# Kernel tuning notes

Measured on AMD Instinct MI355X. Metric: run time of the kernel, lower is better.

The kernel has to match this reference:

```python
import jax, jax.numpy as jnp
import numpy as np
import math

HIDDEN = 1024
HEADS = 16
HEAD_DIM = HIDDEN // HEADS
RANK = 16
LORA_SCALING = 1.0 / RANK  # loralib default lora_alpha=1 -> scaling = alpha/r


def setup_inputs() -> dict:
    key = jax.random.key(0)
    ks = jax.random.split(key, 16)
    bs, seq = 4, 2048
    inp = {
        "hidden_states": jax.random.normal(ks[0], (bs, seq, HIDDEN), dtype=jnp.float32),
        "attention_mask": jnp.zeros((bs, 1, 1, seq), dtype=jnp.float32),
    }
    s = 0.02
    for i, nm in enumerate(["q", "k", "v"]):
        inp[f"W{nm}"] = jax.random.normal(ks[1 + 4 * i], (HIDDEN, HIDDEN), dtype=jnp.float32) * s
        inp[f"b{nm}"] = jnp.zeros((HIDDEN,), dtype=jnp.float32)
        inp[f"A{nm}"] = jax.random.normal(ks[2 + 4 * i], (RANK, HIDDEN), dtype=jnp.float32) * s
        inp[f"B{nm}"] = jnp.zeros((HIDDEN, RANK), dtype=jnp.float32)  # loralib inits B to zero
    return inp


def _lora_linear(x, W, b, A, B):
    # y = x W^T + b + scaling * (x A^T) B^T
    return x @ W.T + b + LORA_SCALING * ((x @ A.T) @ B.T)


def _transform(x, W, b, A, B, bs, seq):
    proj = _lora_linear(x, W, b, A, B)  # [bs, seq, hidden]
    return proj.reshape(bs, seq, HEADS, HEAD_DIM).transpose(0, 2, 1, 3)  # [bs, h, seq, d]


def reference(hidden_states, attention_mask, Wq, bq, Aq, Bq, Wk, bk, Ak, Bk, Wv, bv, Av, Bv):
    bs, seq, _ = hidden_states.shape
    q = _transform(hidden_states, Wq, bq, Aq, Bq, bs, seq)
    k = _transform(hidden_states, Wk, bk, Ak, Bk, bs, seq)
    v = _transform(hidden_states, Wv, bv, Av, Bv, bs, seq)
    scores = jnp.einsum("bhqd,bhkd->bhqk", q, k) / math.sqrt(HEAD_DIM) + attention_mask
    probs = jax.nn.softmax(scores, axis=-1)  # [bs, h, seq, seq]
    out = jnp.einsum("bhqk,bhkd->bhqd", probs, v)  # [bs, h, seq, d]
    return out.transpose(0, 2, 1, 3).reshape(bs, seq, HIDDEN)
```

## Files before the change

### kernel.cpp

```cpp
#include <hip/hip_runtime.h>
#include <stdint.h>

typedef __bf16 bf16x8 __attribute__((ext_vector_type(8)));
typedef float f32x4 __attribute__((ext_vector_type(4)));
typedef float f32x16 __attribute__((ext_vector_type(16)));

static __device__ __forceinline__ unsigned int pk_bf16(float a, float b) {
  unsigned int d;
  asm("v_cvt_pk_bf16_f32 %0, %1, %2" : "=v"(d) : "v"(a), "v"(b));
  return d;
}
static __device__ __forceinline__ float exp2_hw(float x) {
  float r;
  asm("v_exp_f32 %0, %1" : "=v"(r) : "v"(x));
  return r;
}
static __device__ __forceinline__ float rcp_hw(float x) {
  float r;
  asm("v_rcp_f32 %0, %1" : "=v"(r) : "v"(x));
  return r;
}
static __device__ __forceinline__ void gll16(const void* g, void* l) {
  __builtin_amdgcn_global_load_lds((const __attribute__((address_space(1))) unsigned int*)g,
                                   (__attribute__((address_space(3))) unsigned int*)l,
                                   16, 0, 0);
}

__global__ __launch_bounds__(256) void prep_kernel(
    const float* __restrict__ X, unsigned short* __restrict__ Xbf,
    const float* __restrict__ Wq, const float* __restrict__ Aq, const float* __restrict__ Bq,
    const float* __restrict__ Wk, const float* __restrict__ Ak, const float* __restrict__ Bk,
    const float* __restrict__ Wv, const float* __restrict__ Av, const float* __restrict__ Bv,
    unsigned short* __restrict__ Weff) {
  int bid = blockIdx.x;
  if (bid < 8192) {
    int i = (bid * 256 + threadIdx.x) * 4;
    float4 v = *(const float4*)(X + i);
    uint2 o;
    o.x = pk_bf16(v.x, v.y);
    o.y = pk_bf16(v.z, v.w);
    *(uint2*)(Xbf + i) = o;
  } else {
    int idx = ((bid - 8192) * 256 + threadIdx.x) * 4;
    int p = idx >> 20;
    int o = (idx >> 10) & 1023;
    int i = idx & 1023;
    const float* W = (p == 0) ? Wq : (p == 1) ? Wk : Wv;
    const float* A = (p == 0) ? Aq : (p == 1) ? Ak : Av;
    const float* B = (p == 0) ? Bq : (p == 1) ? Bk : Bv;
    float4 acc = {0.f, 0.f, 0.f, 0.f};
#pragma unroll
    for (int r = 0; r < 16; ++r) {
      float bb = B[o * 16 + r];
      float4 av = *(const float4*)&A[r * 1024 + i];
      acc.x += bb * av.x; acc.y += bb * av.y;
      acc.z += bb * av.z; acc.w += bb * av.w;
    }
    float4 wv = *(const float4*)&W[o * 1024 + i];
    uint2 ov;
    ov.x = pk_bf16(wv.x + acc.x * 0.0625f, wv.y + acc.y * 0.0625f);
    ov.y = pk_bf16(wv.z + acc.z * 0.0625f, wv.w + acc.w * 0.0625f);
    *(uint2*)&Weff[idx] = ov;
  }
}

__global__ __launch_bounds__(256) void gemm_qkv(
    const unsigned short* __restrict__ X, const unsigned short* __restrict__ Weff,
    const float* __restrict__ bq, const float* __restrict__ bk, const float* __restrict__ bv,
    unsigned short* __restrict__ qbuf, unsigned short* __restrict__ kbuf,
    unsigned short* __restrict__ vtbuf) {
  __shared__ __align__(16) unsigned short As[2][128][32];
  __shared__ __align__(16) unsigned short Bs[2][128][32];
  const int K = 1024;
  int tid = threadIdx.x;
  int lane = tid & 63;
  int w = tid >> 6;
  int wm = (w >> 1) * 64;
  int wn = (w & 1) * 64;
  int c = lane & 15;
  int quad = lane >> 4;

  int bid0 = blockIdx.x;
  int bid = (bid0 & 7) * 192 + (bid0 >> 3);
  int grp = bid / 192;
  int rem = bid % 192;
  int m0 = (grp * 8 + (rem & 7)) * 128;
  int n0 = (rem >> 3) * 128;
  int p = n0 >> 10;

  int ldr = lane >> 2;
  int ldc = (lane & 3) * 8;
  const unsigned short* gA = X + (m0 + w * 32 + ldr) * K + ldc;
  const unsigned short* gB = Weff + (n0 + w * 32 + ldr) * K + ldc;

  f32x4 acc[4][4] = {};

  if (p == 2) {
    for (int k0 = 0; k0 < K; k0 += 64) {
      __syncthreads();
#pragma unroll
      for (int hh = 0; hh < 2; hh++) {
        gll16(gA + k0 + hh * 32, &As[hh][w * 32][0]);
        gll16(gA + k0 + hh * 32 + 16 * K, &As[hh][w * 32 + 16][0]);
        gll16(gB + k0 + hh * 32, &Bs[hh][w * 32][0]);
        gll16(gB + k0 + hh * 32 + 16 * K, &Bs[hh][w * 32 + 16][0]);
      }
      __syncthreads();
#pragma unroll
      for (int hh = 0; hh < 2; hh++) {
        bf16x8 af[4], bfr[4];
#pragma unroll
        for (int mi = 0; mi < 4; mi++)
          af[mi] = *(const bf16x8*)&As[hh][wm + mi * 16 + c][quad * 8];
#pragma unroll
        for (int ni = 0; ni < 4; ni++)
          bfr[ni] = *(const bf16x8*)&Bs[hh][wn + ni * 16 + c][quad * 8];
#pragma unroll
        for (int mi = 0; mi < 4; mi++)
#pragma unroll
          for (int ni = 0; ni < 4; ni++)
            acc[mi][ni] = __builtin_amdgcn_mfma_f32_16x16x32_bf16(af[mi], bfr[ni], acc[mi][ni], 0, 0, 0);
      }
    }
    const float* bias = bv;
#pragma unroll
    for (int ni = 0; ni < 4; ni++) {
      int o = (n0 + wn + ni * 16 + c) & 1023;
      int h = o >> 6;
      int d = o & 63;
      float bval = bias[o];
#pragma unroll
      for (int mi = 0; mi < 4; mi++) {
        int mbase = m0 + wm + mi * 16 + quad * 4;
        int bb = mbase >> 11;
        int s = mbase & 2047;
        uint2 o4;
        o4.x = pk_bf16(acc[mi][ni][0] + bval, acc[mi][ni][1] + bval);
        o4.y = pk_bf16(acc[mi][ni][2] + bval, acc[mi][ni][3] + bval);
        *(uint2*)&vtbuf[((bb * 16 + h) * 64 + d) * 2048 + s] = o4;
      }
    }
  } else {
    for (int k0 = 0; k0 < K; k0 += 64) {
      __syncthreads();
#pragma unroll
      for (int hh = 0; hh < 2; hh++) {
        gll16(gA + k0 + hh * 32, &As[hh][w * 32][0]);
        gll16(gA + k0 + hh * 32 + 16 * K, &As[hh][w * 32 + 16][0]);
        gll16(gB + k0 + hh * 32, &Bs[hh][w * 32][0]);
        gll16(gB + k0 + hh * 32 + 16 * K, &Bs[hh][w * 32 + 16][0]);
      }
      __syncthreads();
#pragma unroll
      for (int hh = 0; hh < 2; hh++) {
        bf16x8 af[4], bfr[4];
#pragma unroll
        for (int mi = 0; mi < 4; mi++)
          af[mi] = *(const bf16x8*)&As[hh][wm + mi * 16 + c][quad * 8];
#pragma unroll
        for (int ni = 0; ni < 4; ni++)
          bfr[ni] = *(const bf16x8*)&Bs[hh][wn + ni * 16 + c][quad * 8];
#pragma unroll
        for (int mi = 0; mi < 4; mi++)
#pragma unroll
          for (int ni = 0; ni < 4; ni++)
            acc[mi][ni] = __builtin_amdgcn_mfma_f32_16x16x32_bf16(bfr[ni], af[mi], acc[mi][ni], 0, 0, 0);
      }
    }
    const float* bias = (p == 1) ? bk : bq;
    unsigned short* dst = (p == 1) ? kbuf : qbuf;
#pragma unroll
    for (int mi = 0; mi < 4; mi++) {
      int m = m0 + wm + mi * 16 + c;
      int bb = m >> 11;
      int ss = m & 2047;
#pragma unroll
      for (int ni = 0; ni < 4; ni++) {
        int o = (n0 + wn + ni * 16 + quad * 4) & 1023;
        int h = o >> 6;
        int d = o & 63;
        float4 b4 = *(const float4*)&bias[o];
        uint2 o4;
        o4.x = pk_bf16(acc[mi][ni][0] + b4.x, acc[mi][ni][1] + b4.y);
        o4.y = pk_bf16(acc[mi][ni][2] + b4.z, acc[mi][ni][3] + b4.w);
        *(uint2*)&dst[((bb * 16 + h) * 2048 + ss) * 64 + d] = o4;
      }
    }
  }
}

__global__ __launch_bounds__(256, 2) void attn_kernel(
    const unsigned short* __restrict__ qbuf, const unsigned short* __restrict__ kbuf,
    const unsigned short* __restrict__ vtbuf, const float* __restrict__ maskg,
    float* __restrict__ out) {
  __shared__ __align__(16) unsigned short Ks[2][64][72];
  __shared__ __align__(16) unsigned short Vts[2][64][72];
  __shared__ __align__(16) float masks2[2048];
  __shared__ __align__(16) float lrow[256];

  const float SC = 0.125f * 1.4426950408889634f;
  const float L2E = 1.4426950408889634f;

  int tid = threadIdx.x;
  int lane = tid & 63;
  int w = tid >> 6;
  int m31 = lane & 31;
  int hi = lane >> 5;

  int g = blockIdx.x;
  int qt = (g >> 3) & 7;
  int bh = ((g >> 6) << 3) | (g & 7);
  int b = bh >> 4;
  int h = bh & 15;
  int q0 = qt * 256;

  const unsigned short* Qbh = qbuf + bh * (2048 * 64);
  const unsigned short* Kbh = kbuf + bh * (2048 * 64);
  const unsigned short* Vbh = vtbuf + bh * (64 * 2048);

#pragma unroll
  for (int i = 0; i < 2; i++) {
    int idx = (i * 256 + tid) * 4;
    float4 mm = *(const float4*)(maskg + b * 2048 + idx);
    float4 mo;
    mo.x = (mm.x - 8.f) * L2E;
    mo.y = (mm.y - 8.f) * L2E;
    mo.z = (mm.z - 8.f) * L2E;
    mo.w = (mm.w - 8.f) * L2E;
    *(float4*)&masks2[idx] = mo;
  }

  bf16x8 qfr[2][4];
#pragma unroll
  for (int qb = 0; qb < 2; qb++)
#pragma unroll
    for (int ks = 0; ks < 4; ks++)
      qfr[qb][ks] = *(const bf16x8*)(Qbh + (q0 + w * 64 + qb * 32 + m31) * 64 + ks * 16 + hi * 8);

  int r2 = tid >> 3;
  int ch = (tid & 7) * 8;

  {
    uint4 t0 = *(const uint4*)(Kbh + r2 * 64 + ch);
    uint4 t1 = *(const uint4*)(Kbh + (32 + r2) * 64 + ch);
    uint4 t2 = *(const uint4*)(Vbh + r2 * 2048 + ch);
    uint4 t3 = *(const uint4*)(Vbh + (r2 + 32) * 2048 + ch);
    *(uint4*)&Ks[0][r2][ch] = t0;
    *(uint4*)&Ks[0][r2 + 32][ch] = t1;
    *(uint4*)&Vts[0][r2][ch] = t2;
    *(uint4*)&Vts[0][r2 + 32][ch] = t3;
  }
  uint4 pkv0 = *(const uint4*)(Kbh + (64 + r2) * 64 + ch);
  uint4 pkv1 = *(const uint4*)(Kbh + (64 + 32 + r2) * 64 + ch);
  uint4 pkv2 = *(const uint4*)(Vbh + r2 * 2048 + 64 + ch);
  uint4 pkv3 = *(const uint4*)(Vbh + (r2 + 32) * 2048 + 64 + ch);

  __syncthreads();

  float lsum[2] = {0.f, 0.f};
  f32x16 acc_o[2][2] = {};

  for (int t = 0; t < 32; t++) {
    int cur = t & 1;
    int kt = t * 64;

#pragma unroll
    for (int kb = 0; kb < 2; kb++) {
      f32x16 accs[2] = {};
      __builtin_amdgcn_s_setprio(1);
#pragma unroll
      for (int ks = 0; ks < 4; ks++) {
        bf16x8 kf = *(const bf16x8*)&Ks[cur][kb * 32 + m31][ks * 16 + hi * 8];
#pragma unroll
        for (int qb = 0; qb < 2; qb++)
          accs[qb] = __builtin_amdgcn_mfma_f32_32x32x16_bf16(kf, qfr[qb][ks], accs[qb], 0, 0, 0);
      }
      __builtin_amdgcn_s_setprio(0);

      unsigned int up[2][4][2];
#pragma unroll
      for (int gg = 0; gg < 4; gg++) {
        float4 m4 = *(const float4*)&masks2[kt + kb * 32 + gg * 8 + hi * 4];
#pragma unroll
        for (int qb = 0; qb < 2; qb++) {
          float p0 = exp2_hw(fmaf(accs[qb][gg * 4 + 0], SC, m4.x));
          float p1 = exp2_hw(fmaf(accs[qb][gg * 4 + 1], SC, m4.y));
          float p2 = exp2_hw(fmaf(accs[qb][gg * 4 + 2], SC, m4.z));
          float p3 = exp2_hw(fmaf(accs[qb][gg * 4 + 3], SC, m4.w));
          lsum[qb] += (p0 + p1) + (p2 + p3);
          up[qb][gg][0] = pk_bf16(p0, p1);
          up[qb][gg][1] = pk_bf16(p2, p3);
        }
      }

#pragma unroll
      for (int gp = 0; gp < 2; gp++) {
        union { uint4 u; bf16x8 bv8; } pf[2];
#pragma unroll
        for (int qb = 0; qb < 2; qb++) {
          unsigned int a0 = up[qb][gp * 2][0], b0 = up[qb][gp * 2 + 1][0];
          unsigned int a1 = up[qb][gp * 2][1], b1 = up[qb][gp * 2 + 1][1];
          asm("v_permlane32_swap_b32 %0, %1" : "+v"(a0), "+v"(b0));
          asm("v_permlane32_swap_b32 %0, %1" : "+v"(a1), "+v"(b1));
          pf[qb].u.x = a0;
          pf[qb].u.y = a1;
          pf[qb].u.z = b0;
          pf[qb].u.w = b1;
        }
        __builtin_amdgcn_s_setprio(1);
#pragma unroll
        for (int db = 0; db < 2; db++) {
          bf16x8 vf = *(const bf16x8*)&Vts[cur][db * 32 + m31][kb * 32 + gp * 16 + hi * 8];
#pragma unroll
          for (int qb = 0; qb < 2; qb++)
            acc_o[db][qb] = __builtin_amdgcn_mfma_f32_32x32x16_bf16(pf[qb].bv8, vf, acc_o[db][qb], 0, 0, 0);
        }
        __builtin_amdgcn_s_setprio(0);
      }
    }

    if (t < 31) {
      int nb = cur ^ 1;
      *(uint4*)&Ks[nb][r2][ch] = pkv0;
      *(uint4*)&Ks[nb][r2 + 32][ch] = pkv1;
      *(uint4*)&Vts[nb][r2][ch] = pkv2;
      *(uint4*)&Vts[nb][r2 + 32][ch] = pkv3;
      int kn = (kt + 128) & 2047;
      pkv0 = *(const uint4*)(Kbh + (kn + r2) * 64 + ch);
      pkv1 = *(const uint4*)(Kbh + (kn + 32 + r2) * 64 + ch);
      pkv2 = *(const uint4*)(Vbh + r2 * 2048 + kn + ch);
      pkv3 = *(const uint4*)(Vbh + (r2 + 32) * 2048 + kn + ch);
    }
    __syncthreads();
  }

#pragma unroll
  for (int qb = 0; qb < 2; qb++) {
    lsum[qb] += __shfl_xor(lsum[qb], 32);
    lrow[w * 64 + qb * 32 + m31] = lsum[qb];
  }
  __asm__ volatile("" ::: "memory");

#pragma unroll
  for (int qb = 0; qb < 2; qb++)
#pragma unroll
    for (int gg = 0; gg < 4; gg++) {
      float4 l4 = *(const float4*)&lrow[w * 64 + qb * 32 + gg * 8 + hi * 4];
      float i0 = rcp_hw(l4.x), i1 = rcp_hw(l4.y), i2 = rcp_hw(l4.z), i3 = rcp_hw(l4.w);
      int qq = q0 + w * 64 + qb * 32 + gg * 8 + hi * 4;
#pragma unroll
      for (int db = 0; db < 2; db++) {
        float* obase = out + (b * 2048 + qq) * 1024 + h * 64 + db * 32 + m31;
        obase[0 * 1024] = acc_o[db][qb][gg * 4 + 0] * i0;
        obase[1 * 1024] = acc_o[db][qb][gg * 4 + 1] * i1;
        obase[2 * 1024] = acc_o[db][qb][gg * 4 + 2] * i2;
        obase[3 * 1024] = acc_o[db][qb][gg * 4 + 3] * i3;
      }
    }
}

extern "C" void kernel_launch(void* const* d_in, const int* in_sizes, int n_in,
                              void* d_out, int out_size, void* d_ws, size_t ws_size,
                              hipStream_t stream) {
  const float* X    = (const float*)d_in[0];
  const float* mask = (const float*)d_in[1];
  const float* Wq = (const float*)d_in[2];
  const float* bq = (const float*)d_in[3];
  const float* Aq = (const float*)d_in[4];
  const float* Bq = (const float*)d_in[5];
  const float* Wk = (const float*)d_in[6];
  const float* bk = (const float*)d_in[7];
  const float* Ak = (const float*)d_in[8];
  const float* Bk = (const float*)d_in[9];
  const float* Wv = (const float*)d_in[10];
  const float* bv = (const float*)d_in[11];
  const float* Av = (const float*)d_in[12];
  const float* Bv = (const float*)d_in[13];

  unsigned short* ws    = (unsigned short*)d_ws;
  unsigned short* Xbf   = ws;
  unsigned short* Weff  = Xbf + 8388608;
  unsigned short* qbuf  = Weff + 3145728;
  unsigned short* kbuf  = qbuf + 8388608;
  unsigned short* vtbuf = kbuf + 8388608;

  prep_kernel<<<dim3(11264), dim3(256), 0, stream>>>(X, Xbf, Wq, Aq, Bq, Wk, Ak, Bk, Wv, Av, Bv, Weff);
  gemm_qkv<<<dim3(1536), dim3(256), 0, stream>>>(Xbf, Weff, bq, bk, bv, qbuf, kbuf, vtbuf);
  attn_kernel<<<dim3(512), dim3(256), 0, stream>>>(qbuf, kbuf, vtbuf, mask, (float*)d_out);
}
```

Before: 263.3 us.

## Halve per-warp query rows in attention and use 512-thread blocks; drop gemm swizzle

The attention kernel now assigns 32 query rows per warp instead of 64 and launches 8 warps per block, keeping the 256-query tile. The goal is lower register pressure and more resident warps to hide latency. In exchange, each K/V fragment read from LDS feeds only one MFMA, so LDS traffic per FLOP doubles. The GEMM also drops its block-index swizzle and uses the plain linear block order, which changes L2 locality.

```diff
diff --git a/kernel.cpp b/kernel.cpp
--- a/kernel.cpp
+++ b/kernel.cpp
@@ -80,8 +80,7 @@
   int c = lane & 15;
   int quad = lane >> 4;
 
-  int bid0 = blockIdx.x;
-  int bid = (bid0 & 7) * 192 + (bid0 >> 3);
+  int bid = blockIdx.x;
   int grp = bid / 192;
   int rem = bid % 192;
   int m0 = (grp * 8 + (rem & 7)) * 128;
@@ -189,7 +188,7 @@
   }
 }
 
-__global__ __launch_bounds__(256, 2) void attn_kernel(
+__global__ __launch_bounds__(512, 4) void attn_kernel(
     const unsigned short* __restrict__ qbuf, const unsigned short* __restrict__ kbuf,
     const unsigned short* __restrict__ vtbuf, const float* __restrict__ maskg,
     float* __restrict__ out) {
@@ -218,9 +217,8 @@
   const unsigned short* Kbh = kbuf + bh * (2048 * 64);
   const unsigned short* Vbh = vtbuf + bh * (64 * 2048);
 
-#pragma unroll
-  for (int i = 0; i < 2; i++) {
-    int idx = (i * 256 + tid) * 4;
+  {
+    int idx = tid * 4;
     float4 mm = *(const float4*)(maskg + b * 2048 + idx);
     float4 mo;
     mo.x = (mm.x - 8.f) * L2E;
@@ -230,35 +228,27 @@
     *(float4*)&masks2[idx] = mo;
   }
 
-  bf16x8 qfr[2][4];
-#pragma unroll
-  for (int qb = 0; qb < 2; qb++)
-#pragma unroll
-    for (int ks = 0; ks < 4; ks++)
-      qfr[qb][ks] = *(const bf16x8*)(Qbh + (q0 + w * 64 + qb * 32 + m31) * 64 + ks * 16 + hi * 8);
+  bf16x8 qfr[4];
+#pragma unroll
+  for (int ks = 0; ks < 4; ks++)
+    qfr[ks] = *(const bf16x8*)(Qbh + (q0 + w * 32 + m31) * 64 + ks * 16 + hi * 8);
 
   int r2 = tid >> 3;
   int ch = (tid & 7) * 8;
 
   {
     uint4 t0 = *(const uint4*)(Kbh + r2 * 64 + ch);
-    uint4 t1 = *(const uint4*)(Kbh + (32 + r2) * 64 + ch);
     uint4 t2 = *(const uint4*)(Vbh + r2 * 2048 + ch);
-    uint4 t3 = *(const uint4*)(Vbh + (r2 + 32) * 2048 + ch);
     *(uint4*)&Ks[0][r2][ch] = t0;
-    *(uint4*)&Ks[0][r2 + 32][ch] = t1;
     *(uint4*)&Vts[0][r2][ch] = t2;
-    *(uint4*)&Vts[0][r2 + 32][ch] = t3;
   }
   uint4 pkv0 = *(const uint4*)(Kbh + (64 + r2) * 64 + ch);
-  uint4 pkv1 = *(const uint4*)(Kbh + (64 + 32 + r2) * 64 + ch);
   uint4 pkv2 = *(const uint4*)(Vbh + r2 * 2048 + 64 + ch);
-  uint4 pkv3 = *(const uint4*)(Vbh + (r2 + 32) * 2048 + 64 + ch);
 
   __syncthreads();
 
-  float lsum[2] = {0.f, 0.f};
-  f32x16 acc_o[2][2] = {};
+  float lsum = 0.f;
+  f32x16 acc_o[2] = {};
 
   for (int t = 0; t < 32; t++) {
     int cur = t & 1;
@@ -266,54 +256,44 @@
 
 #pragma unroll
     for (int kb = 0; kb < 2; kb++) {
-      f32x16 accs[2] = {};
+      f32x16 accs = {};
       __builtin_amdgcn_s_setprio(1);
 #pragma unroll
       for (int ks = 0; ks < 4; ks++) {
         bf16x8 kf = *(const bf16x8*)&Ks[cur][kb * 32 + m31][ks * 16 + hi * 8];
-#pragma unroll
-        for (int qb = 0; qb < 2; qb++)
-          accs[qb] = __builtin_amdgcn_mfma_f32_32x32x16_bf16(kf, qfr[qb][ks], accs[qb], 0, 0, 0);
+        accs = __builtin_amdgcn_mfma_f32_32x32x16_bf16(kf, qfr[ks], accs, 0, 0, 0);
       }
       __builtin_amdgcn_s_setprio(0);
 
-      unsigned int up[2][4][2];
+      unsigned int up[4][2];
 #pragma unroll
       for (int gg = 0; gg < 4; gg++) {
         float4 m4 = *(const float4*)&masks2[kt + kb * 32 + gg * 8 + hi * 4];
-#pragma unroll
-        for (int qb = 0; qb < 2; qb++) {
-          float p0 = exp2_hw(fmaf(accs[qb][gg * 4 + 0], SC, m4.x));
-          float p1 = exp2_hw(fmaf(accs[qb][gg * 4 + 1], SC, m4.y));
-          float p2 = exp2_hw(fmaf(accs[qb][gg * 4 + 2], SC, m4.z));
-          float p3 = exp2_hw(fmaf(accs[qb][gg * 4 + 3], SC, m4.w));
-          lsum[qb] += (p0 + p1) + (p2 + p3);
-          up[qb][gg][0] = pk_bf16(p0, p1);
-          up[qb][gg][1] = pk_bf16(p2, p3);
-        }
+        float p0 = exp2_hw(fmaf(accs[gg * 4 + 0], SC, m4.x));
+        float p1 = exp2_hw(fmaf(accs[gg * 4 + 1], SC, m4.y));
+        float p2 = exp2_hw(fmaf(accs[gg * 4 + 2], SC, m4.z));
+        float p3 = exp2_hw(fmaf(accs[gg * 4 + 3], SC, m4.w));
+        lsum += (p0 + p1) + (p2 + p3);
+        up[gg][0] = pk_bf16(p0, p1);
+        up[gg][1] = pk_bf16(p2, p3);
       }
 
 #pragma unroll
       for (int gp = 0; gp < 2; gp++) {
-        union { uint4 u; bf16x8 bv8; } pf[2];
-#pragma unroll
-        for (int qb = 0; qb < 2; qb++) {
-          unsigned int a0 = up[qb][gp * 2][0], b0 = up[qb][gp * 2 + 1][0];
-          unsigned int a1 = up[qb][gp * 2][1], b1 = up[qb][gp * 2 + 1][1];
-          asm("v_permlane32_swap_b32 %0, %1" : "+v"(a0), "+v"(b0));
-          asm("v_permlane32_swap_b32 %0, %1" : "+v"(a1), "+v"(b1));
-          pf[qb].u.x = a0;
-          pf[qb].u.y = a1;
-          pf[qb].u.z = b0;
-          pf[qb].u.w = b1;
-        }
+        union { uint4 u; bf16x8 bv8; } pf;
+        unsigned int a0 = up[gp * 2][0], b0 = up[gp * 2 + 1][0];
+        unsigned int a1 = up[gp * 2][1], b1 = up[gp * 2 + 1][1];
+        asm("v_permlane32_swap_b32 %0, %1" : "+v"(a0), "+v"(b0));
+        asm("v_permlane32_swap_b32 %0, %1" : "+v"(a1), "+v"(b1));
+        pf.u.x = a0;
+        pf.u.y = a1;
+        pf.u.z = b0;
+        pf.u.w = b1;
         __builtin_amdgcn_s_setprio(1);
 #pragma unroll
         for (int db = 0; db < 2; db++) {
           bf16x8 vf = *(const bf16x8*)&Vts[cur][db * 32 + m31][kb * 32 + gp * 16 + hi * 8];
-#pragma unroll
-          for (int qb = 0; qb < 2; qb++)
-            acc_o[db][qb] = __builtin_amdgcn_mfma_f32_32x32x16_bf16(pf[qb].bv8, vf, acc_o[db][qb], 0, 0, 0);
+          acc_o[db] = __builtin_amdgcn_mfma_f32_32x32x16_bf16(pf.bv8, vf, acc_o[db], 0, 0, 0);
         }
         __builtin_amdgcn_s_setprio(0);
       }
@@ -322,41 +302,32 @@
     if (t < 31) {
       int nb = cur ^ 1;
       *(uint4*)&Ks[nb][r2][ch] = pkv0;
-      *(uint4*)&Ks[nb][r2 + 32][ch] = pkv1;
       *(uint4*)&Vts[nb][r2][ch] = pkv2;
-      *(uint4*)&Vts[nb][r2 + 32][ch] = pkv3;
       int kn = (kt + 128) & 2047;
       pkv0 = *(const uint4*)(Kbh + (kn + r2) * 64 + ch);
-      pkv1 = *(const uint4*)(Kbh + (kn + 32 + r2) * 64 + ch);
       pkv2 = *(const uint4*)(Vbh + r2 * 2048 + kn + ch);
-      pkv3 = *(const uint4*)(Vbh + (r2 + 32) * 2048 + kn + ch);
     }
     __syncthreads();
   }
 
-#pragma unroll
-  for (int qb = 0; qb < 2; qb++) {
-    lsum[qb] += __shfl_xor(lsum[qb], 32);
-    lrow[w * 64 + qb * 32 + m31] = lsum[qb];
-  }
+  lsum += __shfl_xor(lsum, 32);
+  lrow[w * 32 + m31] = lsum;
   __asm__ volatile("" ::: "memory");
 
 #pragma unroll
-  for (int qb = 0; qb < 2; qb++)
-#pragma unroll
-    for (int gg = 0; gg < 4; gg++) {
-      float4 l4 = *(const float4*)&lrow[w * 64 + qb * 32 + gg * 8 + hi * 4];
-      float i0 = rcp_hw(l4.x), i1 = rcp_hw(l4.y), i2 = rcp_hw(l4.z), i3 = rcp_hw(l4.w);
-      int qq = q0 + w * 64 + qb * 32 + gg * 8 + hi * 4;
-#pragma unroll
-      for (int db = 0; db < 2; db++) {
-        float* obase = out + (b * 2048 + qq) * 1024 + h * 64 + db * 32 + m31;
-        obase[0 * 1024] = acc_o[db][qb][gg * 4 + 0] * i0;
-        obase[1 * 1024] = acc_o[db][qb][gg * 4 + 1] * i1;
-        obase[2 * 1024] = acc_o[db][qb][gg * 4 + 2] * i2;
-        obase[3 * 1024] = acc_o[db][qb][gg * 4 + 3] * i3;
-      }
-    }
+  for (int gg = 0; gg < 4; gg++) {
+    float4 l4 = *(const float4*)&lrow[w * 32 + gg * 8 + hi * 4];
+    float i0 = rcp_hw(l4.x), i1 = rcp_hw(l4.y), i2 = rcp_hw(l4.z), i3 = rcp_hw(l4.w);
+    int qq = q0 + w * 32 + gg * 8 + hi * 4;
+#pragma unroll
+    for (int db = 0; db < 2; db++) {
+      float* obase = out + (b * 2048 + qq) * 1024 + h * 64 + db * 32 + m31;
+      obase[0 * 1024] = acc_o[db][gg * 4 + 0] * i0;
+      obase[1 * 1024] = acc_o[db][gg * 4 + 1] * i1;
+      obase[2 * 1024] = acc_o[db][gg * 4 + 2] * i2;
+      obase[3 * 1024] = acc_o[db][gg * 4 + 3] * i3;
+    }
+  }
 }
 
 extern "C" void kernel_launch(void* const* d_in, const int* in_sizes, int n_in,
@@ -386,5 +357,5 @@
 
   prep_kernel<<<dim3(11264), dim3(256), 0, stream>>>(X, Xbf, Wq, Aq, Bq, Wk, Ak, Bk, Wv, Av, Bv, Weff);
   gemm_qkv<<<dim3(1536), dim3(256), 0, stream>>>(Xbf, Weff, bq, bk, bv, qbuf, kbuf, vtbuf);
-  attn_kernel<<<dim3(512), dim3(256), 0, stream>>>(qbuf, kbuf, vtbuf, mask, (float*)d_out);
-}
+  attn_kernel<<<dim3(512), dim3(512), 0, stream>>>(qbuf, kbuf, vtbuf, mask, (float*)d_out);
+}
```

Result: no change. 264.4 us, median of 2 (+0.4%).
